# Performance work log

Hardware: AMD Instinct MI355X
Metric: run time of the kernel (lower is better)

The kernel has to match this reference:

```python
import jax, jax.numpy as jnp
import numpy as np

BETA = 1.0  # config.beta
B, G, K, E2 = 1024, 512, 128, 128


def setup_inputs() -> dict:
    key = jax.random.key(0)
    k1, k2, k3, k4, k5 = jax.random.split(key, 5)
    s = 0.05
    return {
        "images": jax.random.normal(k1, (B, G), dtype=jnp.float32),
        "wimg": jax.random.normal(k2, (G, K), dtype=jnp.float32) * s,    # project.weight.T
        "wrec": jax.random.normal(k3, (K, E2), dtype=jnp.float32) * s,   # rec.weight.T
        "wrec2": jax.random.normal(k4, (K + 1, E2), dtype=jnp.float32) * s,  # rec2.weight.T
        "wimg2": jax.random.normal(k5, (G, K, K + 1), dtype=jnp.float32) * s,  # img2.weight.T.reshape(K+1,K,G).T
    }


def _soft_assign(x, codes):
    # x: [B, D], codes: [D, C] -> softmax over C of -beta * mean_D (x - codes)^2
    xh = -jnp.mean((x[:, :, None] - codes[None]) ** 2, axis=1) * BETA  # [B, C]
    return jax.nn.softmax(xh, axis=-1)


def reference(images, wimg, wrec, wrec2, wimg2):
    # ---- encode ----
    xp = _soft_assign(images, wimg)            # [B, K]
    lat = xp @ wrec                            # [B, E2]
    xp = _soft_assign(lat, wrec.T)             # [B, K] (codes are wrec.T: [E2, K])
    idx = jnp.argmax(xp, axis=-1)              # [B] hard component
    xwimg = jnp.transpose(wimg2[:, idx, :], (1, 0, 2))   # [B, G, K+1]
    base = wimg[:, idx].T[:, :, None]                     # [B, G, 1]
    xd = images[:, :, None] - base - xwimg                # [B, G, K+1]
    xh2 = -jnp.mean(xd ** 2, axis=1) * BETA               # [B, K+1]
    xp2 = jax.nn.softmax(xh2, axis=-1)
    lat2 = xp2 @ wrec2                                    # [B, E2]
    # ---- decode (ret='rec', n_step>=1) ----
    xp_d = _soft_assign(lat, wrec.T)           # [B, K]
    xp2_d = _soft_assign(lat2, wrec2.T)        # [B, K+1]
    wimgg = wimg[:, :, None] + wimg2           # [G, K, K+1]
    # tensordot(xp_d[:, :, None]*xp2_d[:, None, :], wimgg.permute(1,2,0), 2)
    xrec = jnp.einsum('bk,bj,gkj->bg', xp_d, xp2_d, wimgg)  # [B, G]
    # ---- loss ----
    loss = jnp.mean((xrec - images) ** 2, axis=-1)  # [B]
    return loss
```

## Files before the change

### kernel.cpp

```cpp
#include <hip/hip_runtime.h>

#define B_    1024
#define G_    512
#define K_    128
#define J_    129
#define JP_   132
#define E2_   128
#define KK_   16512
#define KK2_  16896
#define KKE2_ 17024
#define KKP_  17408
#define SPLITS 16
#define KCHUNK 1088
#define BK_   64
#define KSTEPS 17
#define GS_   16

using short8 = __attribute__((ext_vector_type(8))) short;
using f32x4  = __attribute__((ext_vector_type(4))) float;

__device__ __forceinline__ float bf2f(unsigned short h){
  return __uint_as_float(((unsigned int)h) << 16);
}
__device__ __forceinline__ unsigned short f2bf(float f){
  unsigned int u = __float_as_uint(f);
  u += 0x7fffu + ((u >> 16) & 1u);
  return (unsigned short)(u >> 16);
}

#define GLOAD16(gptr, ldst) __builtin_amdgcn_global_load_lds( \
    (const __attribute__((address_space(1))) unsigned int*)(gptr), \
    (__attribute__((address_space(3))) unsigned int*)(ldst), 16, 0, 0)

__device__ __forceinline__ void blockSum2(float v0, float v1, float* red, int t,
                                          float& r0, float& r1){
  #pragma unroll
  for (int off = 32; off > 0; off >>= 1){
    v0 += __shfl_down(v0, off);
    v1 += __shfl_down(v1, off);
  }
  __syncthreads();
  if ((t & 63) == 0){ red[t >> 6] = v0; red[8 + (t >> 6)] = v1; }
  __syncthreads();
  r0 = ((red[0] + red[1]) + (red[2] + red[3])) + ((red[4] + red[5]) + (red[6] + red[7]));
  r1 = ((red[8] + red[9]) + (red[10] + red[11])) + ((red[12] + red[13]) + (red[14] + red[15]));
  __syncthreads();
}

__device__ __forceinline__ void blockSoftmaxMS2(float x0, float x1, bool act,
    float* redm, float* reds, int t,
    float& m0o, float& s0o, float& m1o, float& s1o){
  float m0 = x0, s0 = act ? 1.f : 0.f;
  float m1 = x1, s1 = act ? 1.f : 0.f;
  #pragma unroll
  for (int off = 32; off > 0; off >>= 1){
    float om0 = __shfl_down(m0, off), os0 = __shfl_down(s0, off);
    float om1 = __shfl_down(m1, off), os1 = __shfl_down(s1, off);
    float nm0 = fmaxf(m0, om0);
    s0 = s0*__expf(m0 - nm0) + os0*__expf(om0 - nm0); m0 = nm0;
    float nm1 = fmaxf(m1, om1);
    s1 = s1*__expf(m1 - nm1) + os1*__expf(om1 - nm1); m1 = nm1;
  }
  __syncthreads();
  if ((t & 63) == 0){
    redm[t >> 6] = m0; reds[t >> 6] = s0;
    redm[8 + (t >> 6)] = m1; reds[8 + (t >> 6)] = s1;
  }
  __syncthreads();
  float gm0 = redm[0], gs0 = reds[0], gm1 = redm[8], gs1 = reds[8];
  #pragma unroll
  for (int w = 1; w < 8; w++){
    float om0 = redm[w], os0 = reds[w];
    float nm0 = fmaxf(gm0, om0);
    gs0 = gs0*__expf(gm0 - nm0) + os0*__expf(om0 - nm0); gm0 = nm0;
    float om1 = redm[8 + w], os1 = reds[8 + w];
    float nm1 = fmaxf(gm1, om1);
    gs1 = gs1*__expf(gm1 - nm1) + os1*__expf(om1 - nm1); gm1 = nm1;
  }
  m0o = gm0; s0o = gs0; m1o = gm1; s1o = gs1;
}

__device__ __forceinline__ void blockSoftmaxMSI2(float x0, float x1, int idx, bool act,
    float* redm, float* reds, int* redi, int t,
    float& m0o, float& s0o, int& i0o, float& m1o, float& s1o, int& i1o){
  float m0 = x0, s0 = act ? 1.f : 0.f; int i0 = idx;
  float m1 = x1, s1 = act ? 1.f : 0.f; int i1 = idx;
  #pragma unroll
  for (int off = 32; off > 0; off >>= 1){
    float om0 = __shfl_down(m0, off), os0 = __shfl_down(s0, off);
    int   oi0 = __shfl_down(i0, off);
    float om1 = __shfl_down(m1, off), os1 = __shfl_down(s1, off);
    int   oi1 = __shfl_down(i1, off);
    bool tk0 = (om0 > m0) || (om0 == m0 && oi0 < i0);
    float nm0 = fmaxf(m0, om0);
    s0 = s0*__expf(m0 - nm0) + os0*__expf(om0 - nm0);
    i0 = tk0 ? oi0 : i0; m0 = nm0;
    bool tk1 = (om1 > m1) || (om1 == m1 && oi1 < i1);
    float nm1 = fmaxf(m1, om1);
    s1 = s1*__expf(m1 - nm1) + os1*__expf(om1 - nm1);
    i1 = tk1 ? oi1 : i1; m1 = nm1;
  }
  __syncthreads();
  if ((t & 63) == 0){
    redm[t >> 6] = m0; reds[t >> 6] = s0; redi[t >> 6] = i0;
    redm[8 + (t >> 6)] = m1; reds[8 + (t >> 6)] = s1; redi[8 + (t >> 6)] = i1;
  }
  __syncthreads();
  float gm0 = redm[0], gs0 = reds[0]; int gi0 = redi[0];
  float gm1 = redm[8], gs1 = reds[8]; int gi1 = redi[8];
  #pragma unroll
  for (int w = 1; w < 8; w++){
    { float om = redm[w], os = reds[w]; int oi = redi[w];
      bool tk = (om > gm0) || (om == gm0 && oi < gi0);
      float nm = fmaxf(gm0, om);
      gs0 = gs0*__expf(gm0 - nm) + os*__expf(om - nm);
      gi0 = tk ? oi : gi0; gm0 = nm; }
    { float om = redm[8 + w], os = reds[8 + w]; int oi = redi[8 + w];
      bool tk = (om > gm1) || (om == gm1 && oi < gi1);
      float nm = fmaxf(gm1, om);
      gs1 = gs1*__expf(gm1 - nm) + os*__expf(om - nm);
      gi1 = tk ? oi : gi1; gm1 = nm; }
  }
  m0o = gm0; s0o = gs0; i0o = gi0; m1o = gm1; s1o = gs1; i1o = gi1;
}

__global__ __launch_bounds__(1024) void norms_kernel(
    const float* __restrict__ wimg, const float* __restrict__ wrec,
    const float* __restrict__ wrec2, float* __restrict__ c1norm,
    float* __restrict__ w3norm, float* __restrict__ w6norm,
    float* __restrict__ wrecT, float* __restrict__ wrec2T,
    unsigned short* __restrict__ W2){
  int t = threadIdx.x;
  if (blockIdx.x == 0){
    __shared__ float red[8][128];
    int k = t & 127, sl = t >> 7;
    float s = 0.f;
    int g0 = sl * (G_/8);
    for (int g = g0; g < g0 + G_/8; g++){
      float v = wimg[g*K_ + k]; s += v*v;
    }
    red[sl][k] = s;
    __syncthreads();
    if (t < 128){
      float r = 0.f;
      #pragma unroll
      for (int i = 0; i < 8; i++) r += red[i][t];
      c1norm[t] = r;
    }
  } else if (blockIdx.x == 1){
    int wave = t >> 6, lane = t & 63;
    for (int k = wave; k < K_; k += 16){
      float v0 = wrec[k*E2_ + lane], v1 = wrec[k*E2_ + 64 + lane];
      float s = v0*v0 + v1*v1;
      #pragma unroll
      for (int off = 32; off > 0; off >>= 1) s += __shfl_down(s, off);
      if (lane == 0) w3norm[k] = s;
    }
  } else if (blockIdx.x == 2){
    int wave = t >> 6, lane = t & 63;
    for (int j = wave; j < J_; j += 16){
      float v0 = wrec2[j*E2_ + lane], v1 = wrec2[j*E2_ + 64 + lane];
      float s = v0*v0 + v1*v1;
      #pragma unroll
      for (int off = 32; off > 0; off >>= 1) s += __shfl_down(s, off);
      if (lane == 0) w6norm[j] = s;
    }
  } else if (blockIdx.x == 3){
    for (int n = t; n < K_*E2_; n += 1024){
      int k = n >> 7, e = n & 127;
      wrecT[e*K_ + k] = wrec[n];
    }
  } else if (blockIdx.x == 4){
    for (int n = t; n < J_*E2_; n += 1024){
      int j = n >> 7, e = n & 127;
      wrec2T[e*J_ + j] = wrec2[n];
    }
  } else {
    int g = (blockIdx.x - 5) * 8 + (t >> 7);
    int col = t & 127;
    unsigned short* dst = W2 + (size_t)g * KKP_;
    dst[KK2_ + col]        = f2bf(wimg[g*K_ + col]);
    dst[KKE2_ + col]       = 0;
    dst[KKE2_ + 128 + col] = 0;
    dst[KKE2_ + 256 + col] = 0;
    dst[col*JP_ + 129] = 0;
    dst[col*JP_ + 130] = 0;
    dst[col*JP_ + 131] = 0;
  }
}

__global__ __launch_bounds__(128) void tables_part_kernel(
    const float* __restrict__ wimg2, const float* __restrict__ wimg,
    float* __restrict__ sqp, float* __restrict__ crp,
    unsigned short* __restrict__ W2){
  int n  = blockIdx.x * 128 + threadIdx.x;
  int gs = blockIdx.y;
  int k = n / J_;
  int w2i = n + 3*k;
  float s0=0,s1=0,s2=0,s3=0, c0=0,c1=0,c2=0,c3=0;
  int gbase = gs * (G_/GS_);
  #pragma unroll 2
  for (int g = gbase; g < gbase + G_/GS_; g += 4){
    float w0 = wimg2[(size_t)(g  )*KK_ + n];
    float w1 = wimg2[(size_t)(g+1)*KK_ + n];
    float w2 = wimg2[(size_t)(g+2)*KK_ + n];
    float w3 = wimg2[(size_t)(g+3)*KK_ + n];
    W2[(size_t)(g  )*KKP_ + w2i] = f2bf(w0);
    W2[(size_t)(g+1)*KKP_ + w2i] = f2bf(w1);
    W2[(size_t)(g+2)*KKP_ + w2i] = f2bf(w2);
    W2[(size_t)(g+3)*KKP_ + w2i] = f2bf(w3);
    s0 += w0*w0; s1 += w1*w1; s2 += w2*w2; s3 += w3*w3;
    c0 += wimg[(g  )*K_ + k]*w0;
    c1 += wimg[(g+1)*K_ + k]*w1;
    c2 += wimg[(g+2)*K_ + k]*w2;
    c3 += wimg[(g+3)*K_ + k]*w3;
  }
  sqp[(size_t)gs*KK_ + n] = (s0+s1)+(s2+s3);
  crp[(size_t)gs*KK_ + n] = (c0+c1)+(c2+c3);
}
__global__ __launch_bounds__(128) void tables_reduce_kernel(
    const float* __restrict__ sqp, const float* __restrict__ crp,
    float* __restrict__ sq2, float* __restrict__ cross){
  int n = blockIdx.x * 128 + threadIdx.x;
  float s = 0.f, c = 0.f;
  #pragma unroll
  for (int gs = 0; gs < GS_; gs++){
    s += sqp[(size_t)gs*KK_ + n];
    c += crp[(size_t)gs*KK_ + n];
  }
  sq2[n] = s; cross[n] = c;
}

__global__ __launch_bounds__(512, 4) void encdec_kernel(
    const float* __restrict__ img,  const float* __restrict__ wimg,
    const float* __restrict__ wrec, const float* __restrict__ wrec2,
    const float* __restrict__ wrecT, const float* __restrict__ wrec2T,
    const unsigned short* __restrict__ W2,
    const float* __restrict__ c1norm, const float* __restrict__ w3norm,
    const float* __restrict__ w6norm, const float* __restrict__ sq2,
    const float* __restrict__ cross, unsigned short* __restrict__ Rm){
  __shared__ __align__(16) float simg[2][G_];
  __shared__ float sp[2][K_];
  __shared__ float sqv[2][JP_];
  __shared__ float slat[2][E2_];
  __shared__ float sd1[2][K_];
  __shared__ __align__(16) float sh16a[16][128];
  __shared__ __align__(16) float sh16b[16][128];
  __shared__ float sh4a[4][K_], sh4b[4][K_];
  __shared__ float xtra[4];
  __shared__ float redm[16], reds[16];
  __shared__ int   redi[16];

  int t = threadIdx.x;
  int b0 = blockIdx.x * 2, b1 = b0 + 1;
  int tt = t & 127, q = t >> 7;
  int ll = t & 31, gq = t >> 5;
  int wvid = t >> 6, lane = t & 63;

  simg[0][t] = img[b0*G_ + t];
  simg[1][t] = img[b1*G_ + t];
  __syncthreads();
  float a0 = simg[0][t], a1 = simg[1][t];
  float in0, in1;
  blockSum2(a0*a0, a1*a1, redm, t, in0, in1);

  {
    float p00=0,p01=0,p02=0,p03=0, p10=0,p11=0,p12=0,p13=0;
    int g0 = gq * 32;
    #pragma unroll 8
    for (int g = g0; g < g0 + 32; g++){
      float4 wv = *(const float4*)(wimg + g*K_ + 4*ll);
      float sv0 = simg[0][g], sv1 = simg[1][g];
      p00 += sv0*wv.x; p01 += sv0*wv.y; p02 += sv0*wv.z; p03 += sv0*wv.w;
      p10 += sv1*wv.x; p11 += sv1*wv.y; p12 += sv1*wv.z; p13 += sv1*wv.w;
    }
    float4 st0 = {p00,p01,p02,p03};
    float4 st1 = {p10,p11,p12,p13};
    *(float4*)&sh16a[gq][4*ll] = st0;
    *(float4*)&sh16b[gq][4*ll] = st1;
  }
  __syncthreads();
  float xh10 = -3e38f, xh11 = -3e38f;
  if (t < 128){
    float d0 = 0.f, d1 = 0.f;
    #pragma unroll
    for (int i = 0; i < 16; i++){ d0 += sh16a[i][t]; d1 += sh16b[i][t]; }
    sd1[0][t] = d0; sd1[1][t] = d1;
    xh10 = -(in0 - 2.f*d0 + c1norm[t]) * (1.f/512.f);
    xh11 = -(in1 - 2.f*d1 + c1norm[t]) * (1.f/512.f);
  }
  float m10, s10, m11, s11;
  blockSoftmaxMS2(xh10, xh11, t < 128, redm, reds, t, m10, s10, m11, s11);
  if (t < 128){
    sp[0][t] = __expf(xh10 - m10) / s10;
    sp[1][t] = __expf(xh11 - m11) / s11;
  }
  __syncthreads();

  {
    float l00=0,l01=0, l10=0,l11=0;
    int k0 = q * 32;
    for (int k = k0; k < k0 + 32; k += 2){
      float w0 = wrec[(k  )*E2_ + tt];
      float w1 = wrec[(k+1)*E2_ + tt];
      l00 += sp[0][k]*w0; l01 += sp[0][k+1]*w1;
      l10 += sp[1][k]*w0; l11 += sp[1][k+1]*w1;
    }
    sh4a[q][tt] = l00 + l01;
    sh4b[q][tt] = l10 + l11;
  }
  __syncthreads();
  float lat0 = (sh4a[0][tt] + sh4a[1][tt]) + (sh4a[2][tt] + sh4a[3][tt]);
  float lat1 = (sh4b[0][tt] + sh4b[1][tt]) + (sh4b[2][tt] + sh4b[3][tt]);
  if (q == 0){ slat[0][tt] = lat0; slat[1][tt] = lat1; }
  float ln0, ln1;
  blockSum2((q == 0) ? lat0*lat0 : 0.f, (q == 0) ? lat1*lat1 : 0.f, redm, t, ln0, ln1);

  {
    float l00=0,l01=0, l10=0,l11=0;
    int e0 = q * 32;
    const float* rT = wrecT + tt;
    for (int e = e0; e < e0 + 32; e += 2){
      float w0 = rT[(e  )*K_];
      float w1 = rT[(e+1)*K_];
      l00 += slat[0][e]*w0; l01 += slat[0][e+1]*w1;
      l10 += slat[1][e]*w0; l11 += slat[1][e+1]*w1;
    }
    sh4a[q][tt] = l00 + l01;
    sh4b[q][tt] = l10 + l11;
  }
  __syncthreads();
  float xh30 = -3e38f, xh31 = -3e38f;
  if (t < 128){
    float d30 = (sh4a[0][t] + sh4a[1][t]) + (sh4a[2][t] + sh4a[3][t]);
    float d31 = (sh4b[0][t] + sh4b[1][t]) + (sh4b[2][t] + sh4b[3][t]);
    xh30 = -(ln0 - 2.f*d30 + w3norm[t]) * (1.f/128.f);
    xh31 = -(ln1 - 2.f*d31 + w3norm[t]) * (1.f/128.f);
  }
  float m30, s30, m31, s31; int idx0, idx1;
  blockSoftmaxMSI2(xh30, xh31, tt, t < 128, redm, reds, redi, t,
                   m30, s30, idx0, m31, s31, idx1);
  if (t < 128){
    sp[0][t] = __expf(xh30 - m30) / s30;
    sp[1][t] = __expf(xh31 - m31) / s31;
  }
  float dsq0 = in0 - 2.f*sd1[0][idx0] + c1norm[idx0];
  float dsq1 = in1 - 2.f*sd1[1][idx1] + c1norm[idx1];

  {
    const unsigned short* Wb0 = W2 + (size_t)idx0 * JP_ + 4*ll;
    const unsigned short* Wb1 = W2 + (size_t)idx1 * JP_ + 4*ll;
    float p00=0,p01=0,p02=0,p03=0, p10=0,p11=0,p12=0,p13=0;
    int g0 = gq * 32;
    #pragma unroll 4
    for (int g = g0; g < g0 + 32; g++){
      uint2 w0 = *(const uint2*)(Wb0 + (size_t)g*KKP_);
      uint2 w1 = *(const uint2*)(Wb1 + (size_t)g*KKP_);
      float sv0 = simg[0][g], sv1 = simg[1][g];
      p00 += sv0 * __uint_as_float(w0.x << 16);
      p01 += sv0 * __uint_as_float(w0.x & 0xffff0000u);
      p02 += sv0 * __uint_as_float(w0.y << 16);
      p03 += sv0 * __uint_as_float(w0.y & 0xffff0000u);
      p10 += sv1 * __uint_as_float(w1.x << 16);
      p11 += sv1 * __uint_as_float(w1.x & 0xffff0000u);
      p12 += sv1 * __uint_as_float(w1.y << 16);
      p13 += sv1 * __uint_as_float(w1.y & 0xffff0000u);
    }
    float4 st0 = {p00,p01,p02,p03};
    float4 st1 = {p10,p11,p12,p13};
    *(float4*)&sh16a[gq][4*ll] = st0;
    *(float4*)&sh16b[gq][4*ll] = st1;
  }
  if (wvid < 2){
    int ib = wvid ? idx1 : idx0;
    const float* si = simg[wvid];
    const unsigned short* Wb8 = W2 + (size_t)ib * JP_ + 128;
    float s = 0.f;
    #pragma unroll
    for (int m = 0; m < 8; m++){
      int g = lane + 64*m;
      s += si[g] * bf2f(Wb8[(size_t)g * KKP_]);
    }
    #pragma unroll
    for (int off = 32; off > 0; off >>= 1) s += __shfl_down(s, off);
    if (lane == 0) xtra[wvid] = s;
  }
  __syncthreads();
  float xh20 = -3e38f, xh21 = -3e38f;
  if (t < J_){
    float di0, di1;
    if (t < 128){
      di0 = 0.f; di1 = 0.f;
      #pragma unroll
      for (int i = 0; i < 16; i++){ di0 += sh16a[i][t]; di1 += sh16b[i][t]; }
    } else { di0 = xtra[0]; di1 = xtra[1]; }
    int nb0 = idx0*J_ + t, nb1 = idx1*J_ + t;
    xh20 = -(dsq0 - 2.f*(di0 - cross[nb0]) + sq2[nb0]) * (1.f/512.f);
    xh21 = -(dsq1 - 2.f*(di1 - cross[nb1]) + sq2[nb1]) * (1.f/512.f);
  }
  float m20, s20, m21, s21;
  blockSoftmaxMS2(xh20, xh21, t < J_, redm, reds, t, m20, s20, m21, s21);
  if (t < J_){
    sqv[0][t] = __expf(xh20 - m20) / s20;
    sqv[1][t] = __expf(xh21 - m21) / s21;
  }
  __syncthreads();

  {
    float lv0 = 0.f, lv1 = 0.f;
    int j0 = (q == 0) ? 0 : (q*32 + 1);
    int j1 = q*32 + 33;
    for (int j = j0; j < j1; j++){
      float w = wrec2[j*E2_ + tt];
      lv0 += sqv[0][j]*w; lv1 += sqv[1][j]*w;
    }
    sh4a[q][tt] = lv0;
    sh4b[q][tt] = lv1;
  }
  __syncthreads();
  float l20 = (sh4a[0][tt] + sh4a[1][tt]) + (sh4a[2][tt] + sh4a[3][tt]);
  float l21 = (sh4b[0][tt] + sh4b[1][tt]) + (sh4b[2][tt] + sh4b[3][tt]);
  if (q == 0){ slat[0][tt] = l20; slat[1][tt] = l21; }
  float n20, n21;
  blockSum2((q == 0) ? l20*l20 : 0.f, (q == 0) ? l21*l21 : 0.f, redm, t, n20, n21);

  {
    float l00=0,l01=0, l10=0,l11=0;
    int e0 = q * 32;
    const float* rT = wrec2T + tt;
    for (int e = e0; e < e0 + 32; e += 2){
      float w0 = rT[(e  )*J_];
      float w1 = rT[(e+1)*J_];
      l00 += slat[0][e]*w0; l01 += slat[0][e+1]*w1;
      l10 += slat[1][e]*w0; l11 += slat[1][e+1]*w1;
    }
    sh4a[q][tt] = l00 + l01;
    sh4b[q][tt] = l10 + l11;
  }
  if (wvid < 2){
    const float* sl = slat[wvid];
    float s = sl[lane]*wrec2T[lane*J_ + 128] + sl[lane+64]*wrec2T[(lane+64)*J_ + 128];
    #pragma unroll
    for (int off = 32; off > 0; off >>= 1) s += __shfl_down(s, off);
    if (lane == 0) xtra[2 + wvid] = s;
  }
  __syncthreads();
  float xh60 = -3e38f, xh61 = -3e38f;
  if (t < J_){
    float d60, d61;
    if (t < 128){
      d60 = (sh4a[0][t] + sh4a[1][t]) + (sh4a[2][t] + sh4a[3][t]);
      d61 = (sh4b[0][t] + sh4b[1][t]) + (sh4b[2][t] + sh4b[3][t]);
    } else { d60 = xtra[2]; d61 = xtra[3]; }
    xh60 = -(n20 - 2.f*d60 + w6norm[t]) * (1.f/128.f);
    xh61 = -(n21 - 2.f*d61 + w6norm[t]) * (1.f/128.f);
  }
  float m60, s60, m61, s61;
  blockSoftmaxMS2(xh60, xh61, t < J_, redm, reds, t, m60, s60, m61, s61);
  if (t < J_){
    sqv[0][t] = __expf(xh60 - m60) / s60;
    sqv[1][t] = __expf(xh61 - m61) / s61;
  }
  __syncthreads();

  unsigned int* R0 = (unsigned int*)(Rm + (size_t)b0 * KKP_);
  unsigned int* R1 = (unsigned int*)(Rm + (size_t)b1 * KKP_);
  int k = t / 66;
  int j2 = t - k*66;
  for (int kk2 = t; kk2 < KKP_/2; kk2 += 512){
    float v00 = 0.f, v01 = 0.f, v10 = 0.f, v11 = 0.f;
    if (kk2 < KK2_/2){
      int j = 2*j2;
      float pk0 = sp[0][k], pk1 = sp[1][k];
      bool jo0 = (j < J_), jo1 = (j+1 < J_);
      v00 = jo0 ? pk0 * sqv[0][j]   : 0.f;
      v01 = jo1 ? pk0 * sqv[0][j+1] : 0.f;
      v10 = jo0 ? pk1 * sqv[1][j]   : 0.f;
      v11 = jo1 ? pk1 * sqv[1][j+1] : 0.f;
    } else if (kk2 < KKE2_/2){
      int e = 2*(kk2 - KK2_/2);
      v00 = sp[0][e]; v01 = sp[0][e+1];
      v10 = sp[1][e]; v11 = sp[1][e+1];
    }
    R0[kk2] = (unsigned int)f2bf(v00) | ((unsigned int)f2bf(v01) << 16);
    R1[kk2] = (unsigned int)f2bf(v10) | ((unsigned int)f2bf(v11) << 16);
    j2 += 50;
    if (j2 >= 66){ j2 -= 66; k += 8; } else k += 7;
  }
}

__global__ __launch_bounds__(256) void gemm_kernel(
    const unsigned short* __restrict__ Rm, const unsigned short* __restrict__ W2,
    unsigned short* __restrict__ part){
  __shared__ __align__(16) unsigned int lds[16384];
  auto lds3 = (__attribute__((address_space(3))) unsigned int*)lds;
  int tid = threadIdx.x;
  int l = tid & 63;
  int wv = tid >> 6;
  int wr = (wv >> 1) * 64, wc = (wv & 1) * 64;
  int b0 = blockIdx.y * 128, g0 = blockIdx.x * 128;
  size_t kkbase = (size_t)blockIdx.z * KCHUNK;

  int srow = tid >> 3;
  int cswz = (tid & 7) ^ (srow & 7);
  const unsigned short* ga = Rm + (size_t)(b0 + srow)*KKP_ + kkbase + cswz*8;
  const unsigned short* gb = W2 + (size_t)(g0 + srow)*KKP_ + kkbase + cswz*8;

  int lrow = l & 15, lh = l >> 4, p7 = l & 7;

  f32x4 zero4 = {0.f, 0.f, 0.f, 0.f};
  f32x4 acc[4][4];
  #pragma unroll
  for (int mi = 0; mi < 4; mi++)
    #pragma unroll
    for (int ni = 0; ni < 4; ni++) acc[mi][ni] = zero4;

  auto STAGE = [&](int bb){
    unsigned int base = bb * 8192;
    #pragma unroll
    for (int c = 0; c < 4; c++){
      GLOAD16(ga + (size_t)c*32*KKP_, lds3 + base + c*1024 + wv*256);
      GLOAD16(gb + (size_t)c*32*KKP_, lds3 + base + 4096 + c*1024 + wv*256);
    }
    ga += BK_; gb += BK_;
  };

  STAGE(0);
  int cur = 0;
  for (int s = 0; s < KSTEPS; s++){
    __syncthreads();
    if (s + 1 < KSTEPS) STAGE(cur ^ 1);
    const unsigned int* lA = lds + cur*8192;
    const unsigned int* lB = lA + 4096;
    #pragma unroll
    for (int s2 = 0; s2 < 2; s2++){
      int slot = ((s2 << 2) + lh) ^ p7;
      short8 af[4], bfv[4];
      #pragma unroll
      for (int mi = 0; mi < 4; mi++)
        af[mi] = *(const short8*)(lA + (wr + mi*16 + lrow)*32 + slot*4);
      #pragma unroll
      for (int ni = 0; ni < 4; ni++)
        bfv[ni] = *(const short8*)(lB + (wc + ni*16 + lrow)*32 + slot*4);
      #pragma unroll
      for (int mi = 0; mi < 4; mi++)
        #pragma unroll
        for (int ni = 0; ni < 4; ni++)
          acc[mi][ni] = __builtin_amdgcn_mfma_f32_16x16x32_bf16(af[mi], bfv[ni], acc[mi][ni], 0, 0, 0);
    }
    cur ^= 1;
  }

  unsigned short* P = part + ((size_t)blockIdx.z * B_ + b0) * G_ + g0;
  int rh = (l >> 4) << 2, cl = l & 15;
  #pragma unroll
  for (int mi = 0; mi < 4; mi++)
    #pragma unroll
    for (int ni = 0; ni < 4; ni++)
      #pragma unroll
      for (int r = 0; r < 4; r++){
        int row = wr + mi*16 + rh + r;
        int col = wc + ni*16 + cl;
        P[(size_t)row*G_ + col] = f2bf(acc[mi][ni][r]);
      }
}

__global__ __launch_bounds__(128) void loss_kernel(
    const float* __restrict__ img, const unsigned short* __restrict__ part,
    float* __restrict__ out){
  __shared__ float redf[2];
  int t = threadIdx.x, b = blockIdx.x;
  float x0 = 0.f, x1 = 0.f, x2 = 0.f, x3 = 0.f;
  #pragma unroll
  for (int z = 0; z < SPLITS; z++){
    const unsigned short* pr = part + ((size_t)z*B_ + b)*G_ + 4*t;
    uint2 v = *(const uint2*)pr;
    x0 += __uint_as_float(v.x << 16);
    x1 += __uint_as_float(v.x & 0xffff0000u);
    x2 += __uint_as_float(v.y << 16);
    x3 += __uint_as_float(v.y & 0xffff0000u);
  }
  float4 iv = *(const float4*)(img + (size_t)b*G_ + 4*t);
  float d0 = x0 - iv.x, d1 = x1 - iv.y, d2 = x2 - iv.z, d3 = x3 - iv.w;
  float acc = (d0*d0 + d1*d1) + (d2*d2 + d3*d3);
  #pragma unroll
  for (int off = 32; off > 0; off >>= 1) acc += __shfl_down(acc, off);
  __syncthreads();
  if ((t & 63) == 0) redf[t >> 6] = acc;
  __syncthreads();
  if (t == 0) out[b] = (redf[0] + redf[1]) * (1.f/512.f);
}

extern "C" void kernel_launch(void* const* d_in, const int* in_sizes, int n_in,
                              void* d_out, int out_size, void* d_ws, size_t ws_size,
                              hipStream_t stream){
  (void)in_sizes; (void)n_in; (void)out_size; (void)ws_size;
  const float* img   = (const float*)d_in[0];
  const float* wimg  = (const float*)d_in[1];
  const float* wrec  = (const float*)d_in[2];
  const float* wrec2 = (const float*)d_in[3];
  const float* wimg2 = (const float*)d_in[4];
  float* out = (float*)d_out;

  char* ws = (char*)d_ws;
  size_t off = 0;
  auto alloc = [&](size_t bytes) -> void* {
    void* p = ws + off;
    off += (bytes + 255) & ~(size_t)255;
    return p;
  };
  unsigned short* W2   = (unsigned short*)alloc((size_t)G_ * KKP_ * 2);
  unsigned short* Rm   = (unsigned short*)alloc((size_t)B_ * KKP_ * 2);
  unsigned short* part = (unsigned short*)alloc((size_t)SPLITS * B_ * G_ * 2);
  float* sqp    = (float*)alloc((size_t)GS_ * KK_ * 4);
  float* crp    = (float*)alloc((size_t)GS_ * KK_ * 4);
  float* sq2    = (float*)alloc((size_t)KK_ * 4);
  float* cross  = (float*)alloc((size_t)KK_ * 4);
  float* c1norm = (float*)alloc(K_ * 4);
  float* w3norm = (float*)alloc(K_ * 4);
  float* w6norm = (float*)alloc(J_ * 4);
  float* wrecT  = (float*)alloc((size_t)K_ * E2_ * 4);
  float* wrec2T = (float*)alloc((size_t)J_ * E2_ * 4);

  norms_kernel<<<dim3(69), dim3(1024), 0, stream>>>(wimg, wrec, wrec2, c1norm, w3norm, w6norm, wrecT, wrec2T, W2);
  tables_part_kernel<<<dim3(129, GS_), dim3(128), 0, stream>>>(wimg2, wimg, sqp, crp, W2);
  tables_reduce_kernel<<<dim3(129), dim3(128), 0, stream>>>(sqp, crp, sq2, cross);
  encdec_kernel<<<dim3(512), dim3(512), 0, stream>>>(img, wimg, wrec, wrec2, wrecT, wrec2T, W2,
      c1norm, w3norm, w6norm, sq2, cross, Rm);
  gemm_kernel<<<dim3(4, 8, SPLITS), dim3(256), 0, stream>>>(Rm, W2, part);
  loss_kernel<<<dim3(1024), dim3(128), 0, stream>>>(img, part, out);
}
```

Before: 110.0 us.

## Move first soft-assign projection to split-bf16 MFMA GEMM kernel

The images·wimg projection and the image norms are taken out of the encdec kernel. Inputs and a transposed wimg are split into bf16 hi/lo pairs, and a new MFMA GEMM computes the projection with three products per tile (hi·hi, hi·lo, lo·hi) to keep near-fp32 accuracy. It writes 4 split-G partials that encdec sums. This removes per-block scalar FMA work and redundant wimg reads in encdec, but adds two kernel launches, extra global traffic for the split inputs and partials, and only a 32-block grid for the GEMM.

```diff
diff --git a/kernel.cpp b/kernel.cpp
--- a/kernel.cpp
+++ b/kernel.cpp
@@ -32,21 +32,6 @@
     (const __attribute__((address_space(1))) unsigned int*)(gptr), \
     (__attribute__((address_space(3))) unsigned int*)(ldst), 16, 0, 0)
 
-__device__ __forceinline__ void blockSum2(float v0, float v1, float* red, int t,
-                                          float& r0, float& r1){
-  #pragma unroll
-  for (int off = 32; off > 0; off >>= 1){
-    v0 += __shfl_down(v0, off);
-    v1 += __shfl_down(v1, off);
-  }
-  __syncthreads();
-  if ((t & 63) == 0){ red[t >> 6] = v0; red[8 + (t >> 6)] = v1; }
-  __syncthreads();
-  r0 = ((red[0] + red[1]) + (red[2] + red[3])) + ((red[4] + red[5]) + (red[6] + red[7]));
-  r1 = ((red[8] + red[9]) + (red[10] + red[11])) + ((red[12] + red[13]) + (red[14] + red[15]));
-  __syncthreads();
-}
-
 __device__ __forceinline__ void blockSoftmaxMS2(float x0, float x1, bool act,
     float* redm, float* reds, int t,
     float& m0o, float& s0o, float& m1o, float& s1o){
@@ -78,6 +63,21 @@
     gs1 = gs1*__expf(gm1 - nm1) + os1*__expf(om1 - nm1); gm1 = nm1;
   }
   m0o = gm0; s0o = gs0; m1o = gm1; s1o = gs1;
+}
+
+__device__ __forceinline__ void blockSum2(float v0, float v1, float* red, int t,
+                                          float& r0, float& r1){
+  #pragma unroll
+  for (int off = 32; off > 0; off >>= 1){
+    v0 += __shfl_down(v0, off);
+    v1 += __shfl_down(v1, off);
+  }
+  __syncthreads();
+  if ((t & 63) == 0){ red[t >> 6] = v0; red[8 + (t >> 6)] = v1; }
+  __syncthreads();
+  r0 = ((red[0] + red[1]) + (red[2] + red[3])) + ((red[4] + red[5]) + (red[6] + red[7]));
+  r1 = ((red[8] + red[9]) + (red[10] + red[11])) + ((red[12] + red[13]) + (red[14] + red[15]));
+  __syncthreads();
 }
 
 __device__ __forceinline__ void blockSoftmaxMSI2(float x0, float x1, int idx, bool act,
@@ -129,6 +129,7 @@
     const float* __restrict__ wrec2, float* __restrict__ c1norm,
     float* __restrict__ w3norm, float* __restrict__ w6norm,
     float* __restrict__ wrecT, float* __restrict__ wrec2T,
+    unsigned short* __restrict__ wThi, unsigned short* __restrict__ wTlo,
     unsigned short* __restrict__ W2){
   int t = threadIdx.x;
   if (blockIdx.x == 0){
@@ -175,8 +176,16 @@
       int j = n >> 7, e = n & 127;
       wrec2T[e*J_ + j] = wrec2[n];
     }
+  } else if (blockIdx.x == 5){
+    for (int n = t; n < K_*G_; n += 1024){
+      int k = n >> 9, g = n & 511;
+      float v = wimg[g*K_ + k];
+      unsigned short h = f2bf(v);
+      wThi[n] = h;
+      wTlo[n] = f2bf(v - bf2f(h));
+    }
   } else {
-    int g = (blockIdx.x - 5) * 8 + (t >> 7);
+    int g = (blockIdx.x - 6) * 8 + (t >> 7);
     int col = t & 127;
     unsigned short* dst = W2 + (size_t)g * KKP_;
     dst[KK2_ + col]        = f2bf(wimg[g*K_ + col]);
@@ -187,6 +196,107 @@
     dst[col*JP_ + 130] = 0;
     dst[col*JP_ + 131] = 0;
   }
+}
+
+__global__ __launch_bounds__(128) void splitimg_kernel(
+    const float* __restrict__ img, unsigned short* __restrict__ ihi,
+    unsigned short* __restrict__ ilo, float* __restrict__ inorm){
+  __shared__ float redf[2];
+  int b = blockIdx.x, t = threadIdx.x;
+  float acc = 0.f;
+  #pragma unroll
+  for (int i = 0; i < 4; i++){
+    int g = t + 128*i;
+    float v = img[b*G_ + g];
+    unsigned short h = f2bf(v);
+    ihi[b*G_ + g] = h;
+    ilo[b*G_ + g] = f2bf(v - bf2f(h));
+    acc += v*v;
+  }
+  #pragma unroll
+  for (int off = 32; off > 0; off >>= 1) acc += __shfl_down(acc, off);
+  if ((t & 63) == 0) redf[t >> 6] = acc;
+  __syncthreads();
+  if (t == 0) inorm[b] = redf[0] + redf[1];
+}
+
+__global__ __launch_bounds__(256) void d1gemm_kernel(
+    const unsigned short* __restrict__ ihi, const unsigned short* __restrict__ ilo,
+    const unsigned short* __restrict__ wThi, const unsigned short* __restrict__ wTlo,
+    float* __restrict__ D1p){
+  __shared__ __align__(16) unsigned int lds[16384];
+  auto lds3 = (__attribute__((address_space(3))) unsigned int*)lds;
+  int tid = threadIdx.x;
+  int l = tid & 63;
+  int wv = tid >> 6;
+  int wr = (wv >> 1) * 64, wc = (wv & 1) * 64;
+  int b0 = blockIdx.x * 128;
+  int gb = blockIdx.y * 128;
+
+  int srow = tid >> 3;
+  int cswz = (tid & 7) ^ (srow & 7);
+  const unsigned short* gah = ihi  + (size_t)(b0 + srow)*G_ + gb + cswz*8;
+  const unsigned short* gal = ilo  + (size_t)(b0 + srow)*G_ + gb + cswz*8;
+  const unsigned short* gbh = wThi + (size_t)srow*G_ + gb + cswz*8;
+  const unsigned short* gbl = wTlo + (size_t)srow*G_ + gb + cswz*8;
+
+  int lrow = l & 15, lh = l >> 4, p7 = l & 7;
+
+  f32x4 zero4 = {0.f, 0.f, 0.f, 0.f};
+  f32x4 acc[4][4];
+  #pragma unroll
+  for (int mi = 0; mi < 4; mi++)
+    #pragma unroll
+    for (int ni = 0; ni < 4; ni++) acc[mi][ni] = zero4;
+
+  for (int ks = 0; ks < 2; ks++){
+    __syncthreads();
+    #pragma unroll
+    for (int c = 0; c < 4; c++){
+      GLOAD16(gah + (size_t)c*32*G_, lds3 +         c*1024 + wv*256);
+      GLOAD16(gal + (size_t)c*32*G_, lds3 + 4096  + c*1024 + wv*256);
+      GLOAD16(gbh + (size_t)c*32*G_, lds3 + 8192  + c*1024 + wv*256);
+      GLOAD16(gbl + (size_t)c*32*G_, lds3 + 12288 + c*1024 + wv*256);
+    }
+    gah += BK_; gal += BK_; gbh += BK_; gbl += BK_;
+    __syncthreads();
+    #pragma unroll
+    for (int s2 = 0; s2 < 2; s2++){
+      int slot = ((s2 << 2) + lh) ^ p7;
+      short8 ah[4], al[4], bh[4], bl[4];
+      #pragma unroll
+      for (int mi = 0; mi < 4; mi++){
+        ah[mi] = *(const short8*)(lds +         (wr + mi*16 + lrow)*32 + slot*4);
+        al[mi] = *(const short8*)(lds + 4096  + (wr + mi*16 + lrow)*32 + slot*4);
+      }
+      #pragma unroll
+      for (int ni = 0; ni < 4; ni++){
+        bh[ni] = *(const short8*)(lds + 8192  + (wc + ni*16 + lrow)*32 + slot*4);
+        bl[ni] = *(const short8*)(lds + 12288 + (wc + ni*16 + lrow)*32 + slot*4);
+      }
+      #pragma unroll
+      for (int mi = 0; mi < 4; mi++)
+        #pragma unroll
+        for (int ni = 0; ni < 4; ni++){
+          acc[mi][ni] = __builtin_amdgcn_mfma_f32_16x16x32_bf16(ah[mi], bh[ni], acc[mi][ni], 0, 0, 0);
+          acc[mi][ni] = __builtin_amdgcn_mfma_f32_16x16x32_bf16(ah[mi], bl[ni], acc[mi][ni], 0, 0, 0);
+          acc[mi][ni] = __builtin_amdgcn_mfma_f32_16x16x32_bf16(al[mi], bh[ni], acc[mi][ni], 0, 0, 0);
+        }
+    }
+  }
+
+  float* P = D1p + (size_t)blockIdx.y * B_ * K_ + (size_t)b0 * K_;
+  int rh = (l >> 4) << 2, cl = l & 15;
+  #pragma unroll
+  for (int mi = 0; mi < 4; mi++)
+    #pragma unroll
+    for (int ni = 0; ni < 4; ni++)
+      #pragma unroll
+      for (int r = 0; r < 4; r++){
+        int row = wr + mi*16 + rh + r;
+        int col = wc + ni*16 + cl;
+        P[(size_t)row*K_ + col] = acc[mi][ni][r];
+      }
 }
 
 __global__ __launch_bounds__(128) void tables_part_kernel(
@@ -232,13 +342,14 @@
 }
 
 __global__ __launch_bounds__(512, 4) void encdec_kernel(
-    const float* __restrict__ img,  const float* __restrict__ wimg,
+    const float* __restrict__ img,
     const float* __restrict__ wrec, const float* __restrict__ wrec2,
     const float* __restrict__ wrecT, const float* __restrict__ wrec2T,
     const unsigned short* __restrict__ W2,
     const float* __restrict__ c1norm, const float* __restrict__ w3norm,
     const float* __restrict__ w6norm, const float* __restrict__ sq2,
-    const float* __restrict__ cross, unsigned short* __restrict__ Rm){
+    const float* __restrict__ cross, const float* __restrict__ D1p,
+    const float* __restrict__ inorm, unsigned short* __restrict__ Rm){
   __shared__ __align__(16) float simg[2][G_];
   __shared__ float sp[2][K_];
   __shared__ float sqv[2][JP_];
@@ -259,32 +370,15 @@
 
   simg[0][t] = img[b0*G_ + t];
   simg[1][t] = img[b1*G_ + t];
-  __syncthreads();
-  float a0 = simg[0][t], a1 = simg[1][t];
-  float in0, in1;
-  blockSum2(a0*a0, a1*a1, redm, t, in0, in1);
-
-  {
-    float p00=0,p01=0,p02=0,p03=0, p10=0,p11=0,p12=0,p13=0;
-    int g0 = gq * 32;
-    #pragma unroll 8
-    for (int g = g0; g < g0 + 32; g++){
-      float4 wv = *(const float4*)(wimg + g*K_ + 4*ll);
-      float sv0 = simg[0][g], sv1 = simg[1][g];
-      p00 += sv0*wv.x; p01 += sv0*wv.y; p02 += sv0*wv.z; p03 += sv0*wv.w;
-      p10 += sv1*wv.x; p11 += sv1*wv.y; p12 += sv1*wv.z; p13 += sv1*wv.w;
-    }
-    float4 st0 = {p00,p01,p02,p03};
-    float4 st1 = {p10,p11,p12,p13};
-    *(float4*)&sh16a[gq][4*ll] = st0;
-    *(float4*)&sh16b[gq][4*ll] = st1;
-  }
+  float in0 = inorm[b0], in1 = inorm[b1];
   __syncthreads();
   float xh10 = -3e38f, xh11 = -3e38f;
   if (t < 128){
-    float d0 = 0.f, d1 = 0.f;
-    #pragma unroll
-    for (int i = 0; i < 16; i++){ d0 += sh16a[i][t]; d1 += sh16b[i][t]; }
+    const float* Dp = D1p;
+    float d0 = Dp[b0*K_ + t] + Dp[(size_t)B_*K_ + b0*K_ + t]
+             + Dp[(size_t)2*B_*K_ + b0*K_ + t] + Dp[(size_t)3*B_*K_ + b0*K_ + t];
+    float d1 = Dp[b1*K_ + t] + Dp[(size_t)B_*K_ + b1*K_ + t]
+             + Dp[(size_t)2*B_*K_ + b1*K_ + t] + Dp[(size_t)3*B_*K_ + b1*K_ + t];
     sd1[0][t] = d0; sd1[1][t] = d1;
     xh10 = -(in0 - 2.f*d0 + c1norm[t]) * (1.f/512.f);
     xh11 = -(in1 - 2.f*d1 + c1norm[t]) * (1.f/512.f);
@@ -621,12 +715,21 @@
   float* w6norm = (float*)alloc(J_ * 4);
   float* wrecT  = (float*)alloc((size_t)K_ * E2_ * 4);
   float* wrec2T = (float*)alloc((size_t)J_ * E2_ * 4);
-
-  norms_kernel<<<dim3(69), dim3(1024), 0, stream>>>(wimg, wrec, wrec2, c1norm, w3norm, w6norm, wrecT, wrec2T, W2);
+  unsigned short* ihi  = (unsigned short*)alloc((size_t)B_ * G_ * 2);
+  unsigned short* ilo  = (unsigned short*)alloc((size_t)B_ * G_ * 2);
+  unsigned short* wThi = (unsigned short*)alloc((size_t)K_ * G_ * 2);
+  unsigned short* wTlo = (unsigned short*)alloc((size_t)K_ * G_ * 2);
+  float* D1p   = (float*)alloc((size_t)4 * B_ * K_ * 4);
+  float* inorm = (float*)alloc((size_t)B_ * 4);
+
+  norms_kernel<<<dim3(70), dim3(1024), 0, stream>>>(wimg, wrec, wrec2,
+      c1norm, w3norm, w6norm, wrecT, wrec2T, wThi, wTlo, W2);
+  splitimg_kernel<<<dim3(B_), dim3(128), 0, stream>>>(img, ihi, ilo, inorm);
+  d1gemm_kernel<<<dim3(8, 4), dim3(256), 0, stream>>>(ihi, ilo, wThi, wTlo, D1p);
   tables_part_kernel<<<dim3(129, GS_), dim3(128), 0, stream>>>(wimg2, wimg, sqp, crp, W2);
   tables_reduce_kernel<<<dim3(129), dim3(128), 0, stream>>>(sqp, crp, sq2, cross);
-  encdec_kernel<<<dim3(512), dim3(512), 0, stream>>>(img, wimg, wrec, wrec2, wrecT, wrec2T, W2,
-      c1norm, w3norm, w6norm, sq2, cross, Rm);
+  encdec_kernel<<<dim3(512), dim3(512), 0, stream>>>(img, wrec, wrec2, wrecT, wrec2T, W2,
+      c1norm, w3norm, w6norm, sq2, cross, D1p, inorm, Rm);
   gemm_kernel<<<dim3(4, 8, SPLITS), dim3(256), 0, stream>>>(Rm, W2, part);
   loss_kernel<<<dim3(1024), dim3(128), 0, stream>>>(img, part, out);
 }
```

Result: slower. 130.9 us (+19.0%).
